# Optimization experiments

Hardware: AMD Instinct MI355X
Metric: run time of the kernel (lower is better)

## Reference

```python
import jax, jax.numpy as jnp
import numpy as np

BETA = 0.25


def setup_inputs() -> dict:
    key = jax.random.key(0)
    k1, k2 = jax.random.split(key)
    z_e = jax.random.normal(k1, (16, 256, 2048), dtype=jnp.float32)   # [B, C, L]
    # nn.Embedding weight initialized uniform(-1, 1): [num_codewords, codebook_dim]
    emb = jax.random.uniform(k2, (2048, 256), dtype=jnp.float32, minval=-1.0, maxval=1.0)
    return {"z_e": z_e, "emb": emb}


def reference(z_e, emb):
    C = emb.shape[1]
    # Faithful to the torch code: permute(2,1,0) -> [L, C, B], then view(-1, C)
    z = jnp.transpose(z_e, (2, 1, 0))          # [L, C, B]
    flat = z.reshape(-1, C)                    # [N, C] where N = L*C*B / C
    d = (jnp.sum(flat * flat, axis=1, keepdims=True)
         + jnp.sum(emb * emb, axis=1)
         - 2.0 * flat @ emb.T)                 # [N, K]
    indices = jnp.argmin(d, axis=1)            # [N]
    quantized = emb[indices].reshape(z.shape)  # [L, C, B]
    sg = jax.lax.stop_gradient
    vq_loss = (jnp.mean((sg(quantized) - z) ** 2)
               + BETA * jnp.mean((quantized - sg(z)) ** 2))
    return quantized, indices, vq_loss
```

## Files before the change

kernel.cpp:

```cpp
#include <hip/hip_runtime.h>


#define ZE_CL   (256 * 2048)
#define NROWS   32768
#define KC      2048
#define DD      256
#define IDX_OFF 8388608
#define LOSS_OFF (8388608 + 32768)
#define D2 8e-3f

typedef __bf16 bf16x4 __attribute__((ext_vector_type(4)));
typedef __bf16 bf16x8 __attribute__((ext_vector_type(8)));
typedef float  f32x4  __attribute__((ext_vector_type(4)));

#define EN_OFF  0u
#define EH_OFF  8192u
#define EL_OFF  (EH_OFF + 1048576u)
#define AH_OFF  (EL_OFF + 1048576u)
#define AL_OFF  (AH_OFF + 16777216u)
#define CNT_OFF (AL_OFF + 16777216u)
#define LST_OFF (CNT_OFF + 16u)
#define WS_NEED (LST_OFF + 131072u)

static __device__ inline void gld_lds16(const void* g, void* l) {
    __builtin_amdgcn_global_load_lds(
        (const __attribute__((address_space(1))) void*)g,
        (__attribute__((address_space(3))) void*)l, 16, 0, 0);
}

__global__ void vq_prep_emb(const float* __restrict__ emb, float* __restrict__ enorm,
                            __bf16* __restrict__ Eh, __bf16* __restrict__ El) {
    int col = blockIdx.x * 256 + threadIdx.x;
    const float4* src = (const float4*)(emb + (size_t)col * DD);
    int t8 = col >> 8, g = (col >> 4) & 15, c = col & 15;
    float s = 0.f;
#pragma unroll
    for (int ch = 0; ch < 8; ++ch) {
#pragma unroll
        for (int q = 0; q < 4; ++q) {
            float4 v0 = src[ch * 8 + q * 2];
            float4 v1 = src[ch * 8 + q * 2 + 1];
            float f[8] = {v0.x, v0.y, v0.z, v0.w, v1.x, v1.y, v1.z, v1.w};
            bf16x8 h, l;
#pragma unroll
            for (int j = 0; j < 8; ++j) {
                h[j] = (__bf16)f[j];
                l[j] = (__bf16)(f[j] - (float)h[j]);
                s += f[j] * f[j];
            }
            size_t off = ((size_t)(t8 * 8 + ch) * 16384) + (size_t)(g * 1024 + q * 256 + c * 16);
            *(bf16x8*)((char*)Eh + off) = h;
            *(bf16x8*)((char*)El + off) = l;
        }
    }
    enorm[col] = s;
}

__global__ void vq_transpose_split(const float* __restrict__ ze, float* __restrict__ A,
                                   __bf16* __restrict__ Ah, __bf16* __restrict__ Al) {
    __shared__ float T[16 * 272];
    int tid = threadIdx.x;
    int m  = blockIdx.x & 15;
    int lt = blockIdx.x >> 4;
    int l0 = lt * 16;
#pragma unroll
    for (int it = 0; it < 4; ++it) {
        int p   = tid + it * 256;
        int b   = p >> 6;
        int clo = (p >> 2) & 15;
        int l4  = p & 3;
        const float* g = ze + (size_t)b * ZE_CL + (size_t)(m * 16 + clo) * 2048 + l0 + 4 * l4;
        float4 v = *(const float4*)g;
        int jp = 17 * clo + b;
        T[(4 * l4 + 0) * 272 + jp] = v.x;
        T[(4 * l4 + 1) * 272 + jp] = v.y;
        T[(4 * l4 + 2) * 272 + jp] = v.z;
        T[(4 * l4 + 3) * 272 + jp] = v.w;
    }
    __syncthreads();
#pragma unroll
    for (int it = 0; it < 4; ++it) {
        int p  = tid + it * 256;
        int ll = p >> 6;
        int c4 = p & 63;
        int j0 = 4 * c4;
        int base = ll * 272 + 17 * (j0 >> 4) + (j0 & 15);
        float4 v;
        v.x = T[base + 0]; v.y = T[base + 1]; v.z = T[base + 2]; v.w = T[base + 3];
        int n = (l0 + ll) * 16 + m;
        *(float4*)(A + (size_t)n * DD + j0) = v;
        if (Ah) {
            float a0 = -2.f * v.x, a1 = -2.f * v.y, a2 = -2.f * v.z, a3 = -2.f * v.w;
            bf16x4 h, l;
            h[0] = (__bf16)a0; l[0] = (__bf16)(a0 - (float)h[0]);
            h[1] = (__bf16)a1; l[1] = (__bf16)(a1 - (float)h[1]);
            h[2] = (__bf16)a2; l[2] = (__bf16)(a2 - (float)h[2]);
            h[3] = (__bf16)a3; l[3] = (__bf16)(a3 - (float)h[3]);
            int bn = n >> 6, mi = (n >> 4) & 3, r = n & 15;
            int ch = j0 >> 5, q = (j0 >> 3) & 3, hb = (j0 & 7) * 2;
            size_t off = (size_t)bn * 32768 + (size_t)((mi * 8 + ch) * 1024 + q * 256 + r * 16 + hb);
            *(bf16x4*)((char*)Ah + off) = h;
            *(bf16x4*)((char*)Al + off) = l;
        }
    }
}

__global__ __launch_bounds__(256, 2) void vq_main_mfma(
    const __bf16* __restrict__ Ah, const __bf16* __restrict__ Al,
    const __bf16* __restrict__ Eh, const __bf16* __restrict__ El,
    const float* __restrict__ enorm, const float* __restrict__ emb,
    float* out, int* __restrict__ rcount, int* __restrict__ rlist)
{
    __shared__ __align__(16) __bf16 sB[16384];
    __shared__ float sRv[256], sR2[256];
    __shared__ int   sRi[256];
    __shared__ int   sIdx[64], sFlag[64];
    __shared__ float wsum[4];

    const int tid  = threadIdx.x;
    const int wv   = tid >> 6;
    const int lane = tid & 63;
    const int l15  = lane & 15;
    const int quad = lane >> 4;
    const int n0   = blockIdx.x * 64;

    const char* AhB = (const char*)Ah + (size_t)blockIdx.x * 32768;
    const char* AlB = (const char*)Al + (size_t)blockIdx.x * 32768;

    float v1[16], v2[16]; int i1[16];
#pragma unroll
    for (int s = 0; s < 16; ++s) { v1[s] = 3.4e38f; v2[s] = 3.4e38f; i1[s] = 0; }

    for (int nt = 0; nt < 8; ++nt) {
        const char* EhT = (const char*)Eh + (size_t)nt * (8 * 16384);
        const char* ElT = (const char*)El + (size_t)nt * (8 * 16384);
        f32x4 acc[4][4];
#pragma unroll
        for (int a = 0; a < 4; ++a)
#pragma unroll
            for (int b = 0; b < 4; ++b) acc[a][b] = (f32x4){0.f, 0.f, 0.f, 0.f};

        for (int ch = 0; ch < 8; ++ch) {
            __syncthreads();
            {
                const char* srcH = EhT + ch * 16384;
                const char* srcL = ElT + ch * 16384;
#pragma unroll
                for (int it = 0; it < 4; ++it) {
                    int off = (it * 4 + wv) * 1024;
                    gld_lds16(srcH + off + lane * 16, (char*)sB + off);
                    gld_lds16(srcL + off + lane * 16, (char*)sB + 16384 + off);
                }
            }
            bf16x8 ah[4], al[4];
#pragma unroll
            for (int mi = 0; mi < 4; ++mi) {
                size_t off = (size_t)((mi * 8 + ch) * 1024 + quad * 256 + l15 * 16);
                ah[mi] = *(const bf16x8*)(AhB + off);
                al[mi] = *(const bf16x8*)(AlB + off);
            }
            __syncthreads();
            bf16x8 bh[4], bl[4];
#pragma unroll
            for (int nj = 0; nj < 4; ++nj) {
                int boff = (wv * 4 + nj) * 1024 + quad * 256 + l15 * 16;
                bh[nj] = *(const bf16x8*)((const char*)sB + boff);
                bl[nj] = *(const bf16x8*)((const char*)sB + 16384 + boff);
            }
#pragma unroll
            for (int mi = 0; mi < 4; ++mi)
#pragma unroll
                for (int nj = 0; nj < 4; ++nj)
                    acc[mi][nj] = __builtin_amdgcn_mfma_f32_16x16x32_bf16(ah[mi], bh[nj], acc[mi][nj], 0, 0, 0);
#pragma unroll
            for (int mi = 0; mi < 4; ++mi)
#pragma unroll
                for (int nj = 0; nj < 4; ++nj)
                    acc[mi][nj] = __builtin_amdgcn_mfma_f32_16x16x32_bf16(ah[mi], bl[nj], acc[mi][nj], 0, 0, 0);
#pragma unroll
            for (int mi = 0; mi < 4; ++mi)
#pragma unroll
                for (int nj = 0; nj < 4; ++nj)
                    acc[mi][nj] = __builtin_amdgcn_mfma_f32_16x16x32_bf16(al[mi], bh[nj], acc[mi][nj], 0, 0, 0);
        }
#pragma unroll
        for (int nj = 0; nj < 4; ++nj) {
            int k = nt * 256 + wv * 64 + nj * 16 + l15;
            float en = enorm[k];
#pragma unroll
            for (int mi = 0; mi < 4; ++mi)
#pragma unroll
                for (int r = 0; r < 4; ++r) {
                    float d = acc[mi][nj][r] + en;
                    int slot = mi * 4 + r;
                    float nv2 = fminf(v2[slot], fmaxf(v1[slot], d));
                    if (d < v1[slot]) i1[slot] = k;
                    v1[slot] = fminf(v1[slot], d);
                    v2[slot] = nv2;
                }
        }
    }

#pragma unroll
    for (int slot = 0; slot < 16; ++slot) {
        float a1 = v1[slot], a2 = v2[slot];
        int ai = i1[slot];
#pragma unroll
        for (int m = 1; m < 16; m <<= 1) {
            float b1 = __shfl_xor(a1, m, 64);
            float b2 = __shfl_xor(a2, m, 64);
            int bi = __shfl_xor(ai, m, 64);
            float n2 = fminf(fminf(a2, b2), fmaxf(a1, b1));
            if (b1 < a1) ai = bi;
            a1 = fminf(a1, b1);
            a2 = n2;
        }
        if (l15 == 0) {
            int row = (slot >> 2) * 16 + quad * 4 + (slot & 3);
            sRv[row * 4 + wv] = a1;
            sR2[row * 4 + wv] = a2;
            sRi[row * 4 + wv] = ai;
        }
    }
    __syncthreads();
    if (tid < 64) {
        float a1 = sRv[tid * 4], a2 = sR2[tid * 4];
        int ai = sRi[tid * 4];
#pragma unroll
        for (int w2 = 1; w2 < 4; ++w2) {
            float b1 = sRv[tid * 4 + w2], b2 = sR2[tid * 4 + w2];
            int bi = sRi[tid * 4 + w2];
            float n2 = fminf(fminf(a2, b2), fmaxf(a1, b1));
            if (b1 < a1) ai = bi;
            a1 = fminf(a1, b1);
            a2 = n2;
        }
        int fg = (a2 - a1 < D2) ? 1 : 0;
        sIdx[tid] = ai;
        sFlag[tid] = fg;
        out[IDX_OFF + n0 + tid] = (float)ai;
        if (fg) { int p = atomicAdd(rcount, 1); rlist[p] = n0 + tid; }
    }
    __syncthreads();

    float lacc = 0.f;
#pragma unroll
    for (int it = 0; it < 16; ++it) {
        int p = tid + it * 256;
        int r = p >> 6;
        int c4 = p & 63;
        if (!sFlag[r]) {
            int k = sIdx[r];
            size_t off = (size_t)(n0 + r) * DD + 4 * c4;
            float4 q = *(const float4*)(emb + (size_t)k * DD + 4 * c4);
            float4 a = *(const float4*)(out + off);
            float dx = q.x - a.x, dy = q.y - a.y, dz = q.z - a.z, dw = q.w - a.w;
            lacc += dx * dx + dy * dy + dz * dz + dw * dw;
            *(float4*)(out + off) = q;
        }
    }
#pragma unroll
    for (int off = 32; off > 0; off >>= 1) lacc += __shfl_down(lacc, off, 64);
    if ((tid & 63) == 0) wsum[tid >> 6] = lacc;
    __syncthreads();
    if (tid == 0) {
        float bs = wsum[0] + wsum[1] + wsum[2] + wsum[3];
        atomicAdd(out + LOSS_OFF, bs * (1.25f / 8388608.0f));
    }
}

__global__ void vq_rescore(const float* __restrict__ emb, const float* __restrict__ enorm,
                           float* out, const int* __restrict__ rcount,
                           const int* __restrict__ rlist) {
    __shared__ float sX[256];
    __shared__ float sV[256];
    __shared__ int   sK[256];
    __shared__ float sP[256];
    int cnt = *rcount;
    int tid = threadIdx.x;
    for (int li = blockIdx.x; li < cnt; li += gridDim.x) {
        int row = rlist[li];
        __syncthreads();
        sX[tid] = out[(size_t)row * DD + tid];
        __syncthreads();
        float bv = 3.4e38f; int bk = 0;
        for (int jj = 0; jj < 8; ++jj) {
            int k = jj * 256 + tid;
            const float4* e4 = (const float4*)(emb + (size_t)k * DD);
            float dot = 0.f;
#pragma unroll 8
            for (int d4 = 0; d4 < 64; ++d4) {
                float4 e = e4[d4];
                float4 x = *(const float4*)(sX + d4 * 4);
                dot += x.x * e.x + x.y * e.y + x.z * e.z + x.w * e.w;
            }
            float s = enorm[k] - 2.f * dot;
            if (s < bv) { bv = s; bk = k; }
        }
        sV[tid] = bv; sK[tid] = bk;
        __syncthreads();
#pragma unroll
        for (int s = 128; s > 0; s >>= 1) {
            if (tid < s) {
                float vo = sV[tid + s]; int ko = sK[tid + s];
                if (vo < sV[tid] || (vo == sV[tid] && ko < sK[tid])) { sV[tid] = vo; sK[tid] = ko; }
            }
            __syncthreads();
        }
        int k = sK[0];
        float x = sX[tid];
        float q = emb[(size_t)k * DD + tid];
        out[(size_t)row * DD + tid] = q;
        float d = q - x;
        sP[tid] = d * d;
        __syncthreads();
#pragma unroll
        for (int s = 128; s > 0; s >>= 1) {
            if (tid < s) sP[tid] += sP[tid + s];
            __syncthreads();
        }
        if (tid == 0) {
            out[IDX_OFF + row] = (float)k;
            atomicAdd(out + LOSS_OFF, sP[0] * (1.25f / 8388608.0f));
        }
    }
}

__global__ __launch_bounds__(256, 2) void vq_main_f32(const float* __restrict__ emb,
                                                      const float* __restrict__ enorm,
                                                      float* out) {
    const int SA = 68, SE = 68;
    __shared__ float smem[64 * 68 + 64 * 68];
    __shared__ int   sIdx[64];
    __shared__ float wsum[4];
    float* sA = smem;
    float* sEb = smem + 64 * SA;
    float* redv = sEb;
    int*   redi = (int*)(sEb + 64 * 16);
    int tid = threadIdx.x;
    int n0 = blockIdx.x * 64;
    int rg = tid & 15;
    int kg = tid >> 4;
    float minv[4]; int mini[4];
#pragma unroll
    for (int i = 0; i < 4; ++i) { minv[i] = 3.4e38f; mini[i] = 0; }
    const float* A = out;
    for (int kt = 0; kt < KC / 64; ++kt) {
        int k0 = kt * 64;
        float acc[4][4];
#pragma unroll
        for (int i = 0; i < 4; ++i)
#pragma unroll
            for (int j = 0; j < 4; ++j) acc[i][j] = 0.f;
        for (int dc = 0; dc < 4; ++dc) {
            int d0 = dc * 64;
            __syncthreads();
#pragma unroll
            for (int it = 0; it < 4; ++it) {
                int p = tid + it * 256, r = p >> 4, c4 = p & 15;
                *(float4*)(sA + r * SA + 4 * c4) =
                    *(const float4*)(A + (size_t)(n0 + r) * DD + d0 + 4 * c4);
            }
#pragma unroll
            for (int it = 0; it < 4; ++it) {
                int p = tid + it * 256, r = p >> 4, c4 = p & 15;
                *(float4*)(sEb + r * SE + 4 * c4) =
                    *(const float4*)(emb + (size_t)(k0 + r) * DD + d0 + 4 * c4);
            }
            __syncthreads();
#pragma unroll
            for (int d4 = 0; d4 < 16; ++d4) {
                float4 av[4], ev[4];
#pragma unroll
                for (int i = 0; i < 4; ++i) av[i] = *(const float4*)(sA + (rg + 16 * i) * SA + 4 * d4);
#pragma unroll
                for (int j = 0; j < 4; ++j) ev[j] = *(const float4*)(sEb + (kg + 16 * j) * SE + 4 * d4);
#pragma unroll
                for (int i = 0; i < 4; ++i)
#pragma unroll
                    for (int j = 0; j < 4; ++j)
                        acc[i][j] += av[i].x * ev[j].x + av[i].y * ev[j].y +
                                     av[i].z * ev[j].z + av[i].w * ev[j].w;
            }
        }
#pragma unroll
        for (int j = 0; j < 4; ++j) {
            int k = k0 + kg + 16 * j;
            float en = enorm[k];
#pragma unroll
            for (int i = 0; i < 4; ++i) {
                float s = en - 2.f * acc[i][j];
                if (s < minv[i]) { minv[i] = s; mini[i] = k; }
            }
        }
    }
    __syncthreads();
#pragma unroll
    for (int i = 0; i < 4; ++i) {
        int r = rg + 16 * i;
        redv[r * 16 + kg] = minv[i];
        redi[r * 16 + kg] = mini[i];
    }
    __syncthreads();
    if (tid < 64) {
        float bv = redv[tid * 16]; int bi = redi[tid * 16];
        for (int t = 1; t < 16; ++t) {
            float v = redv[tid * 16 + t]; int ii = redi[tid * 16 + t];
            if (v < bv || (v == bv && ii < bi)) { bv = v; bi = ii; }
        }
        sIdx[tid] = bi;
        out[IDX_OFF + n0 + tid] = (float)bi;
    }
    __syncthreads();
    float lacc = 0.f;
#pragma unroll
    for (int it = 0; it < 16; ++it) {
        int p = tid + it * 256, r = p >> 6, c4 = p & 63;
        int k = sIdx[r];
        size_t off = (size_t)(n0 + r) * DD + 4 * c4;
        float4 q = *(const float4*)(emb + (size_t)k * DD + 4 * c4);
        float4 a = *(const float4*)(out + off);
        float dx = q.x - a.x, dy = q.y - a.y, dz = q.z - a.z, dw = q.w - a.w;
        lacc += dx * dx + dy * dy + dz * dz + dw * dw;
        *(float4*)(out + off) = q;
    }
#pragma unroll
    for (int off = 32; off > 0; off >>= 1) lacc += __shfl_down(lacc, off, 64);
    if ((tid & 63) == 0) wsum[tid >> 6] = lacc;
    __syncthreads();
    if (tid == 0) {
        float bs = wsum[0] + wsum[1] + wsum[2] + wsum[3];
        atomicAdd(out + LOSS_OFF, bs * (1.25f / 8388608.0f));
    }
}

extern "C" void kernel_launch(void* const* d_in, const int* in_sizes, int n_in,
                              void* d_out, int out_size, void* d_ws, size_t ws_size,
                              hipStream_t stream) {
    (void)in_sizes; (void)n_in; (void)out_size;
    const float* ze  = (const float*)d_in[0];
    const float* emb = (const float*)d_in[1];
    float* out = (float*)d_out;
    char*  ws  = (char*)d_ws;
    float* enorm = (float*)(ws + EN_OFF);

    hipMemsetAsync((char*)d_out + (size_t)LOSS_OFF * 4, 0, 4, stream);

    if (ws_size >= (size_t)WS_NEED) {
        __bf16* Eh = (__bf16*)(ws + EH_OFF);
        __bf16* El = (__bf16*)(ws + EL_OFF);
        __bf16* Ah = (__bf16*)(ws + AH_OFF);
        __bf16* Al = (__bf16*)(ws + AL_OFF);
        int* rcount = (int*)(ws + CNT_OFF);
        int* rlist  = (int*)(ws + LST_OFF);
        hipMemsetAsync(ws + CNT_OFF, 0, 16, stream);
        vq_prep_emb<<<8, 256, 0, stream>>>(emb, enorm, Eh, El);
        vq_transpose_split<<<2048, 256, 0, stream>>>(ze, out, Ah, Al);
        vq_main_mfma<<<NROWS / 64, 256, 0, stream>>>(Ah, Al, Eh, El, enorm, emb, out, rcount, rlist);
        vq_rescore<<<64, 256, 0, stream>>>(emb, enorm, out, rcount, rlist);
    } else {
        {
        }
        vq_prep_emb<<<8, 256, 0, stream>>>(emb, enorm, (__bf16*)(ws + EH_OFF), (__bf16*)(ws + EH_OFF));
        vq_transpose_split<<<2048, 256, 0, stream>>>(ze, out, (__bf16*)0, (__bf16*)0);
        vq_main_f32<<<NROWS / 64, 256, 0, stream>>>(emb, enorm, out);
    }
}
```

Measured before the change: 308.2 us.

## Double-buffer codebook LDS tiles, drop fp32 transpose write, widen embedding prep

The main MFMA kernel now double-buffers the codebook tiles in LDS. It prefetches the next tile with global_load_lds while computing on the current one, which removes one barrier per chunk. The transpose kernel no longer writes the fp32 transposed input to the output buffer. The loss now reconstructs x from the bf16 hi/lo split, and the rescore pass reads rows straight from z_e, which saves a 32 MB write and read. Embedding prep uses 8x more threads with a shuffle reduction. The costs are twice the LDS per block (possible occupancy loss) and a loss computed from the split values rather than exact fp32.

```diff
diff --git a/kernel.cpp b/kernel.cpp
--- a/kernel.cpp
+++ b/kernel.cpp
@@ -30,33 +30,48 @@
 
 __global__ void vq_prep_emb(const float* __restrict__ emb, float* __restrict__ enorm,
                             __bf16* __restrict__ Eh, __bf16* __restrict__ El) {
-    int col = blockIdx.x * 256 + threadIdx.x;
-    const float4* src = (const float4*)(emb + (size_t)col * DD);
+    int tid = threadIdx.x;
+    int col = blockIdx.x * 32 + (tid >> 3);
+    int ch  = tid & 7;
+    const float4* src = (const float4*)(emb + (size_t)col * DD) + ch * 8;
     int t8 = col >> 8, g = (col >> 4) & 15, c = col & 15;
     float s = 0.f;
 #pragma unroll
-    for (int ch = 0; ch < 8; ++ch) {
-#pragma unroll
-        for (int q = 0; q < 4; ++q) {
-            float4 v0 = src[ch * 8 + q * 2];
-            float4 v1 = src[ch * 8 + q * 2 + 1];
-            float f[8] = {v0.x, v0.y, v0.z, v0.w, v1.x, v1.y, v1.z, v1.w};
-            bf16x8 h, l;
-#pragma unroll
-            for (int j = 0; j < 8; ++j) {
-                h[j] = (__bf16)f[j];
-                l[j] = (__bf16)(f[j] - (float)h[j]);
-                s += f[j] * f[j];
-            }
-            size_t off = ((size_t)(t8 * 8 + ch) * 16384) + (size_t)(g * 1024 + q * 256 + c * 16);
-            *(bf16x8*)((char*)Eh + off) = h;
-            *(bf16x8*)((char*)El + off) = l;
-        }
-    }
-    enorm[col] = s;
-}
-
-__global__ void vq_transpose_split(const float* __restrict__ ze, float* __restrict__ A,
+    for (int q = 0; q < 4; ++q) {
+        float4 v0 = src[q * 2];
+        float4 v1 = src[q * 2 + 1];
+        float f[8] = {v0.x, v0.y, v0.z, v0.w, v1.x, v1.y, v1.z, v1.w};
+        bf16x8 h, l;
+#pragma unroll
+        for (int j = 0; j < 8; ++j) {
+            h[j] = (__bf16)f[j];
+            l[j] = (__bf16)(f[j] - (float)h[j]);
+            s += f[j] * f[j];
+        }
+        size_t off = ((size_t)(t8 * 8 + ch) * 16384) + (size_t)(g * 1024 + q * 256 + c * 16);
+        *(bf16x8*)((char*)Eh + off) = h;
+        *(bf16x8*)((char*)El + off) = l;
+    }
+    s += __shfl_down(s, 4, 8);
+    s += __shfl_down(s, 2, 8);
+    s += __shfl_down(s, 1, 8);
+    if (ch == 0) enorm[col] = s;
+}
+
+__global__ void vq_enorm(const float* __restrict__ emb, float* __restrict__ enorm) {
+    int k = blockIdx.x * blockDim.x + threadIdx.x;
+    if (k >= KC) return;
+    const float4* e4 = (const float4*)(emb + (size_t)k * DD);
+    float s = 0.f;
+#pragma unroll
+    for (int i = 0; i < DD / 4; ++i) {
+        float4 v = e4[i];
+        s += v.x * v.x + v.y * v.y + v.z * v.z + v.w * v.w;
+    }
+    enorm[k] = s;
+}
+
+__global__ void vq_transpose_split(const float* __restrict__ ze, float* __restrict__ Aout,
                                    __bf16* __restrict__ Ah, __bf16* __restrict__ Al) {
     __shared__ float T[16 * 272];
     int tid = threadIdx.x;
@@ -88,7 +103,7 @@
         float4 v;
         v.x = T[base + 0]; v.y = T[base + 1]; v.z = T[base + 2]; v.w = T[base + 3];
         int n = (l0 + ll) * 16 + m;
-        *(float4*)(A + (size_t)n * DD + j0) = v;
+        if (Aout) *(float4*)(Aout + (size_t)n * DD + j0) = v;
         if (Ah) {
             float a0 = -2.f * v.x, a1 = -2.f * v.y, a2 = -2.f * v.z, a3 = -2.f * v.w;
             bf16x4 h, l;
@@ -111,7 +126,7 @@
     const float* __restrict__ enorm, const float* __restrict__ emb,
     float* out, int* __restrict__ rcount, int* __restrict__ rlist)
 {
-    __shared__ __align__(16) __bf16 sB[16384];
+    __shared__ __align__(16) __bf16 sB[32768];
     __shared__ float sRv[256], sR2[256];
     __shared__ int   sRi[256];
     __shared__ int   sIdx[64], sFlag[64];
@@ -131,9 +146,18 @@
 #pragma unroll
     for (int s = 0; s < 16; ++s) { v1[s] = 3.4e38f; v2[s] = 3.4e38f; i1[s] = 0; }
 
+    {
+        const char* srcH = (const char*)Eh;
+        const char* srcL = (const char*)El;
+#pragma unroll
+        for (int it = 0; it < 4; ++it) {
+            int off = (it * 4 + wv) * 1024;
+            gld_lds16(srcH + off + lane * 16, (char*)sB + off);
+            gld_lds16(srcL + off + lane * 16, (char*)sB + 16384 + off);
+        }
+    }
+
     for (int nt = 0; nt < 8; ++nt) {
-        const char* EhT = (const char*)Eh + (size_t)nt * (8 * 16384);
-        const char* ElT = (const char*)El + (size_t)nt * (8 * 16384);
         f32x4 acc[4][4];
 #pragma unroll
         for (int a = 0; a < 4; ++a)
@@ -141,15 +165,18 @@
             for (int b = 0; b < 4; ++b) acc[a][b] = (f32x4){0.f, 0.f, 0.f, 0.f};
 
         for (int ch = 0; ch < 8; ++ch) {
+            const int t = nt * 8 + ch;
+            const int p = t & 1;
             __syncthreads();
-            {
-                const char* srcH = EhT + ch * 16384;
-                const char* srcL = ElT + ch * 16384;
+            if (t < 63) {
+                const char* srcH = (const char*)Eh + (size_t)(t + 1) * 16384;
+                const char* srcL = (const char*)El + (size_t)(t + 1) * 16384;
+                char* dst = (char*)sB + (1 - p) * 32768;
 #pragma unroll
                 for (int it = 0; it < 4; ++it) {
                     int off = (it * 4 + wv) * 1024;
-                    gld_lds16(srcH + off + lane * 16, (char*)sB + off);
-                    gld_lds16(srcL + off + lane * 16, (char*)sB + 16384 + off);
+                    gld_lds16(srcH + off + lane * 16, dst + off);
+                    gld_lds16(srcL + off + lane * 16, dst + 16384 + off);
                 }
             }
             bf16x8 ah[4], al[4];
@@ -159,13 +186,13 @@
                 ah[mi] = *(const bf16x8*)(AhB + off);
                 al[mi] = *(const bf16x8*)(AlB + off);
             }
-            __syncthreads();
+            const char* buf = (const char*)sB + p * 32768;
             bf16x8 bh[4], bl[4];
 #pragma unroll
             for (int nj = 0; nj < 4; ++nj) {
                 int boff = (wv * 4 + nj) * 1024 + quad * 256 + l15 * 16;
-                bh[nj] = *(const bf16x8*)((const char*)sB + boff);
-                bl[nj] = *(const bf16x8*)((const char*)sB + 16384 + boff);
+                bh[nj] = *(const bf16x8*)(buf + boff);
+                bl[nj] = *(const bf16x8*)(buf + 16384 + boff);
             }
 #pragma unroll
             for (int mi = 0; mi < 4; ++mi)
@@ -239,24 +266,32 @@
         sIdx[tid] = ai;
         sFlag[tid] = fg;
         out[IDX_OFF + n0 + tid] = (float)ai;
-        if (fg) { int p = atomicAdd(rcount, 1); rlist[p] = n0 + tid; }
+        if (fg) { int pq = atomicAdd(rcount, 1); rlist[pq] = n0 + tid; }
     }
     __syncthreads();
 
     float lacc = 0.f;
 #pragma unroll
     for (int it = 0; it < 16; ++it) {
-        int p = tid + it * 256;
-        int r = p >> 6;
-        int c4 = p & 63;
+        int pp = tid + it * 256;
+        int r  = pp >> 6;
+        int c4 = pp & 63;
         if (!sFlag[r]) {
+            int j0 = 4 * c4;
+            int mi = r >> 4, r16 = r & 15;
+            int ch = j0 >> 5, q4i = (j0 >> 3) & 3, hb = (j0 & 7) * 2;
+            size_t aoff = (size_t)((mi * 8 + ch) * 1024 + q4i * 256 + r16 * 16 + hb);
+            bf16x4 h = *(const bf16x4*)(AhB + aoff);
+            bf16x4 l = *(const bf16x4*)(AlB + aoff);
             int k = sIdx[r];
-            size_t off = (size_t)(n0 + r) * DD + 4 * c4;
-            float4 q = *(const float4*)(emb + (size_t)k * DD + 4 * c4);
-            float4 a = *(const float4*)(out + off);
-            float dx = q.x - a.x, dy = q.y - a.y, dz = q.z - a.z, dw = q.w - a.w;
+            float4 q = *(const float4*)(emb + (size_t)k * DD + j0);
+            float x0 = -0.5f * ((float)h[0] + (float)l[0]);
+            float x1 = -0.5f * ((float)h[1] + (float)l[1]);
+            float x2 = -0.5f * ((float)h[2] + (float)l[2]);
+            float x3 = -0.5f * ((float)h[3] + (float)l[3]);
+            float dx = q.x - x0, dy = q.y - x1, dz = q.z - x2, dw = q.w - x3;
             lacc += dx * dx + dy * dy + dz * dz + dw * dw;
-            *(float4*)(out + off) = q;
+            *(float4*)(out + (size_t)(n0 + r) * DD + j0) = q;
         }
     }
 #pragma unroll
@@ -269,9 +304,9 @@
     }
 }
 
-__global__ void vq_rescore(const float* __restrict__ emb, const float* __restrict__ enorm,
-                           float* out, const int* __restrict__ rcount,
-                           const int* __restrict__ rlist) {
+__global__ void vq_rescore(const float* __restrict__ ze, const float* __restrict__ emb,
+                           const float* __restrict__ enorm, float* out,
+                           const int* __restrict__ rcount, const int* __restrict__ rlist) {
     __shared__ float sX[256];
     __shared__ float sV[256];
     __shared__ int   sK[256];
@@ -281,7 +316,8 @@
     for (int li = blockIdx.x; li < cnt; li += gridDim.x) {
         int row = rlist[li];
         __syncthreads();
-        sX[tid] = out[(size_t)row * DD + tid];
+        sX[tid] = ze[(size_t)(tid & 15) * ZE_CL +
+                     (size_t)((row & 15) * 16 + (tid >> 4)) * 2048 + (row >> 4)];
         __syncthreads();
         float bv = 3.4e38f; int bk = 0;
         for (int jj = 0; jj < 8; ++jj) {
@@ -454,14 +490,12 @@
         int* rcount = (int*)(ws + CNT_OFF);
         int* rlist  = (int*)(ws + LST_OFF);
         hipMemsetAsync(ws + CNT_OFF, 0, 16, stream);
-        vq_prep_emb<<<8, 256, 0, stream>>>(emb, enorm, Eh, El);
-        vq_transpose_split<<<2048, 256, 0, stream>>>(ze, out, Ah, Al);
+        vq_prep_emb<<<64, 256, 0, stream>>>(emb, enorm, Eh, El);
+        vq_transpose_split<<<2048, 256, 0, stream>>>(ze, (float*)0, Ah, Al);
         vq_main_mfma<<<NROWS / 64, 256, 0, stream>>>(Ah, Al, Eh, El, enorm, emb, out, rcount, rlist);
-        vq_rescore<<<64, 256, 0, stream>>>(emb, enorm, out, rcount, rlist);
+        vq_rescore<<<64, 256, 0, stream>>>(ze, emb, enorm, out, rcount, rlist);
     } else {
-        {
-        }
-        vq_prep_emb<<<8, 256, 0, stream>>>(emb, enorm, (__bf16*)(ws + EH_OFF), (__bf16*)(ws + EH_OFF));
+        vq_enorm<<<KC / 256, 256, 0, stream>>>(emb, enorm);
         vq_transpose_split<<<2048, 256, 0, stream>>>(ze, out, (__bf16*)0, (__bf16*)0);
         vq_main_f32<<<NROWS / 64, 256, 0, stream>>>(emb, enorm, out);
     }
```

New measurement: 417.2 us. 1.35x slower.
